# Kernel optimization log

Hardware: AMD Instinct MI355X
Metric: run time of the kernel (lower is better)

## Reference

```python
import jax, jax.numpy as jnp
import numpy as np

N = 16384          # num nodes (adj is dense NxN)
INPUT_DIM = 512
HIDDEN = 128
E_POS = 524288
E_NEG = 524288


def setup_inputs() -> dict:
    key = jax.random.key(0)
    k1, k2, k3, k4, k5, k6, k7 = jax.random.split(key, 7)
    X = jax.random.normal(k1, (N, INPUT_DIM), dtype=jnp.float32)
    adj = jax.random.uniform(k2, (N, N), dtype=jnp.float32)
    train_edges = jax.random.randint(k3, (E_POS, 2), 0, N, dtype=jnp.int64)
    train_false_edges = jax.random.randint(k4, (E_NEG, 2), 0, N, dtype=jnp.int64)
    # parameters (xavier / kaiming scale approximated with uniform bounds)
    b1 = float(np.sqrt(6.0 / (INPUT_DIM + HIDDEN)))
    weight = jax.random.uniform(k5, (INPUT_DIM, HIDDEN), minval=-b1, maxval=b1, dtype=jnp.float32)
    b2 = float(np.sqrt(6.0 / (2 * HIDDEN + HIDDEN)))
    weight_two = jax.random.uniform(k6, (2 * HIDDEN, HIDDEN), minval=-b2, maxval=b2, dtype=jnp.float32)
    b3 = float(np.sqrt(6.0 / HIDDEN) / np.sqrt(2.0))  # kaiming_uniform a=1
    weight_three = jax.random.uniform(k7, (HIDDEN, 1), minval=-b3, maxval=b3, dtype=jnp.float32)
    return {"X": X, "adj": adj, "weight": weight, "weight_two": weight_two,
            "weight_three": weight_three, "train_edges": train_edges,
            "train_false_edges": train_false_edges}


def reference(X, adj, weight, weight_two, weight_three, train_edges, train_false_edges):
    # encode: Z = adj @ (X @ W)
    Z = adj @ (X @ weight)                                  # [N, H]
    edges = jnp.concatenate([train_edges, train_false_edges], axis=0)  # [E, 2]
    # decode: vectorized gather-concat replacing the per-edge Python loop
    z_pair = jnp.concatenate([Z[edges[:, 0]], Z[edges[:, 1]]], axis=1)  # [E, 2H]
    h = jax.nn.relu(z_pair) @ weight_two @ weight_three      # [E, 1]
    return jax.nn.sigmoid(h)
```

## Files before the change

### kernel.cpp

```cpp
#include <hip/hip_runtime.h>


#define N_NODES 16384
#define IN_DIM  512
#define HID     128
#define E_POS_N 524288
#define E_TOT   1048576

typedef __bf16 bf16x8 __attribute__((ext_vector_type(8)));
typedef float  f32x4  __attribute__((ext_vector_type(4)));
typedef unsigned short us8 __attribute__((ext_vector_type(8)));
typedef unsigned short us4 __attribute__((ext_vector_type(4)));

__device__ __forceinline__ bf16x8 ldsb(const void* p){
  return __builtin_bit_cast(bf16x8, *reinterpret_cast<const us8*>(p));
}
__device__ __forceinline__ void gload16(const void* g, void* l){
  __builtin_amdgcn_global_load_lds(
      (const __attribute__((address_space(1))) unsigned int*)g,
      (__attribute__((address_space(3))) unsigned int*)l, 16, 0, 0);
}
__device__ __forceinline__ void gload16nt(const void* g, void* l){
  __builtin_amdgcn_global_load_lds(
      (const __attribute__((address_space(1))) unsigned int*)g,
      (__attribute__((address_space(3))) unsigned int*)l, 16, 0, 2);
}

__device__ __forceinline__ void split8(const float* f, bf16x8& hi, bf16x8& lo){
  unsigned u[8];
#pragma unroll
  for (int i = 0; i < 8; ++i) u[i] = __float_as_uint(f[i]);
  uint4 hv;
  hv.x = __builtin_amdgcn_perm(u[1], u[0], 0x07060302u);
  hv.y = __builtin_amdgcn_perm(u[3], u[2], 0x07060302u);
  hv.z = __builtin_amdgcn_perm(u[5], u[4], 0x07060302u);
  hv.w = __builtin_amdgcn_perm(u[7], u[6], 0x07060302u);
  hi = __builtin_bit_cast(bf16x8, hv);
  bf16x8 lv;
#pragma unroll
  for (int i = 0; i < 8; ++i)
    lv[i] = (__bf16)(f[i] - __uint_as_float(u[i] & 0xFFFF0000u));
  lo = lv;
}

__global__ __launch_bounds__(512) void prep_kernel(const float* __restrict__ W,
                                                   const float* __restrict__ w2,
                                                   const float* __restrict__ w3,
                                                   unsigned short* __restrict__ bfW,
                                                   float* __restrict__ w23){
  const int blk = blockIdx.x, tid = threadIdx.x;
  if (blk < 16){
    const int c = tid & 127, g = tid >> 7;
    float f[8];
#pragma unroll
    for (int j = 0; j < 8; ++j) f[j] = W[(blk * 32 + g * 8 + j) * HID + c];
    bf16x8 hi, lo; split8(f, hi, lo);
    const int sw = (c & 7) << 4;
    char* tb = (char*)bfW + blk * 16384 + c * 128;
    *(us8*)(tb + ((g * 16) ^ sw))      = __builtin_bit_cast(us8, hi);
    *(us8*)(tb + ((64 + g * 16) ^ sw)) = __builtin_bit_cast(us8, lo);
  } else if (tid < 256){
    float acc = 0.f;
#pragma unroll 4
    for (int k = 0; k < HID; ++k) acc = fmaf(w2[tid * HID + k], w3[k], acc);
    w23[tid] = acc;
  }
}

__global__ __launch_bounds__(256) void xw_kernel(const float* __restrict__ X,
                                                 const unsigned short* __restrict__ bfW,
                                                 unsigned short* __restrict__ bfB){
  __shared__ alignas(16) char lds[4][24576];
  const int tid = threadIdx.x, lane = tid & 63, w = tid >> 6;
  const int blk = blockIdx.x;
  const int g = lane >> 4, l15 = lane & 15;

  int aoff[4][2], boffH[2], boffL[2];
#pragma unroll
  for (int m = 0; m < 4; ++m){
    const int r = m * 16 + l15, sw = (r & 7) << 4;
    aoff[m][0] = r * 128 + ((g * 32) ^ sw);
    aoff[m][1] = r * 128 + ((g * 32 + 16) ^ sw);
  }
#pragma unroll
  for (int n = 0; n < 2; ++n){
    const int c = (w & 3) * 32 + n * 16 + l15, sw = (c & 7) << 4;
    boffH[n] = 8192 + c * 128 + ((g * 16) ^ sw);
    boffL[n] = 8192 + c * 128 + ((64 + g * 16) ^ sw);
  }

  const char* xsrc[2];
#pragma unroll
  for (int i = 0; i < 2; ++i){
    const int r = i * 32 + (tid >> 3);
    xsrc[i] = (const char*)X + ((size_t)(blk * 64 + r) * IN_DIM) * 4
            + (((tid & 7) * 16) ^ ((r & 7) << 4));
  }
  const char* bsrc = (const char*)bfW + tid * 16;

#define XSTAGE(buf, tt) do { \
    gload16(xsrc[0] + (tt) * 128, (buf) + tid * 16); \
    gload16(xsrc[1] + (tt) * 128, (buf) + 4096 + tid * 16); \
    gload16(bsrc + (size_t)(tt) * 16384,         (buf) + 8192  + tid * 16); \
    gload16(bsrc + (size_t)(tt) * 16384 + 4096,  (buf) + 12288 + tid * 16); \
    gload16(bsrc + (size_t)(tt) * 16384 + 8192,  (buf) + 16384 + tid * 16); \
    gload16(bsrc + (size_t)(tt) * 16384 + 12288, (buf) + 20480 + tid * 16); \
  } while (0)

  f32x4 acc[4][2] = {};
  auto compute = [&](const char* bp){
    bf16x8 bHv[2], bLv[2];
#pragma unroll
    for (int n = 0; n < 2; ++n){ bHv[n] = ldsb(bp + boffH[n]); bLv[n] = ldsb(bp + boffL[n]); }
#pragma unroll
    for (int m = 0; m < 4; ++m){
      f32x4 v0 = *(const f32x4*)(bp + aoff[m][0]);
      f32x4 v1 = *(const f32x4*)(bp + aoff[m][1]);
      float f[8] = {v0[0], v0[1], v0[2], v0[3], v1[0], v1[1], v1[2], v1[3]};
      bf16x8 aH, aL; split8(f, aH, aL);
      __builtin_amdgcn_s_setprio(1);
#pragma unroll
      for (int n = 0; n < 2; ++n) acc[m][n] = __builtin_amdgcn_mfma_f32_16x16x32_bf16(aH, bHv[n], acc[m][n], 0, 0, 0);
#pragma unroll
      for (int n = 0; n < 2; ++n) acc[m][n] = __builtin_amdgcn_mfma_f32_16x16x32_bf16(aH, bLv[n], acc[m][n], 0, 0, 0);
#pragma unroll
      for (int n = 0; n < 2; ++n) acc[m][n] = __builtin_amdgcn_mfma_f32_16x16x32_bf16(aL, bHv[n], acc[m][n], 0, 0, 0);
      __builtin_amdgcn_s_setprio(0);
    }
  };

  XSTAGE(lds[0], 0); XSTAGE(lds[1], 1); XSTAGE(lds[2], 2);
  asm volatile("s_waitcnt vmcnt(12)" ::: "memory");
  __builtin_amdgcn_s_barrier();

  const int nt = IN_DIM / 32;
#pragma unroll 1
  for (int t = 0; t < nt; ++t){
    char* bp = lds[t & 3];
    if (t + 3 < nt) XSTAGE(lds[(t + 3) & 3], t + 3);
    compute(bp);
    if (t + 3 < nt)      asm volatile("s_waitcnt vmcnt(12)" ::: "memory");
    else if (t + 2 < nt) asm volatile("s_waitcnt vmcnt(6)" ::: "memory");
    else if (t + 1 < nt) asm volatile("s_waitcnt vmcnt(0)" ::: "memory");
    if (t + 1 < nt) __builtin_amdgcn_s_barrier();
  }
#undef XSTAGE

#pragma unroll
  for (int m = 0; m < 4; ++m){
#pragma unroll
    for (int n = 0; n < 2; ++n){
      const int col = (w & 3) * 32 + n * 16 + l15;
      const int T   = 2 * blk + (m >> 1);
      const int g2  = (2 * m + (g >> 1)) & 3;
      const int sw  = (col & 7) << 4;
      char* tb = (char*)bfB + (size_t)T * 16384 + col * 128;
      uint2 hv;
      hv.x = __builtin_amdgcn_perm(__float_as_uint(acc[m][n][1]), __float_as_uint(acc[m][n][0]), 0x07060302u);
      hv.y = __builtin_amdgcn_perm(__float_as_uint(acc[m][n][3]), __float_as_uint(acc[m][n][2]), 0x07060302u);
      us4 lv;
#pragma unroll
      for (int j = 0; j < 4; ++j){
        unsigned u = __float_as_uint(acc[m][n][j]);
        lv[j] = __builtin_bit_cast(unsigned short,
                 (__bf16)(acc[m][n][j] - __uint_as_float(u & 0xFFFF0000u)));
      }
      *(uint2*)(tb + (((g2 * 16) ^ sw) + (g & 1) * 8))      = hv;
      *(uint2*)(tb + (((64 + g2 * 16) ^ sw) + (g & 1) * 8)) = __builtin_bit_cast(uint2, lv);
    }
  }
}

__global__ __launch_bounds__(512, 4) void zgemm_kernel(const float* __restrict__ adj,
                                                       const unsigned short* __restrict__ bfB,
                                                       float* __restrict__ part){
  __shared__ alignas(16) char lds[2][32768];
  const int tid = threadIdx.x, lane = tid & 63, w = tid >> 6;
  const int wm = w >> 1, wn = w & 1;
  const int xcd = blockIdx.x & 7;
  const int s   = xcd & 3;
  const int mt  = ((xcd >> 2) << 6) + (blockIdx.x >> 3);
  const int k0  = s * (N_NODES / 4);
  const int nt  = (N_NODES / 4) / 32;
  const int g = lane >> 4, l15 = lane & 15;

  int aoff[2][2], boffH[4], boffL[4];
#pragma unroll
  for (int m = 0; m < 2; ++m){
    const int r = wm * 32 + m * 16 + l15, sw = (r & 7) << 4;
    aoff[m][0] = r * 128 + ((g * 32) ^ sw);
    aoff[m][1] = r * 128 + ((g * 32 + 16) ^ sw);
  }
#pragma unroll
  for (int n = 0; n < 4; ++n){
    const int c = wn * 64 + n * 16 + l15, sw = (c & 7) << 4;
    boffH[n] = 16384 + c * 128 + ((g * 16) ^ sw);
    boffL[n] = 16384 + c * 128 + ((64 + g * 16) ^ sw);
  }

  const char* asrc[2];
#pragma unroll
  for (int i = 0; i < 2; ++i){
    const int r = i * 64 + (tid >> 3);
    asrc[i] = (const char*)adj + ((size_t)(mt * 128 + r) * N_NODES + k0) * 4
            + (((tid & 7) * 16) ^ ((r & 7) << 4));
  }
  const char* bsrc = (const char*)bfB + (size_t)(k0 >> 5) * 16384 + tid * 16;

#define ZSTAGE(buf, tt) do { \
    gload16nt(asrc[0] + (size_t)(tt) * 128, (buf) + tid * 16); \
    gload16nt(asrc[1] + (size_t)(tt) * 128, (buf) + 8192 + tid * 16); \
    gload16(bsrc + (size_t)(tt) * 16384,        (buf) + 16384 + tid * 16); \
    gload16(bsrc + (size_t)(tt) * 16384 + 8192, (buf) + 24576 + tid * 16); \
  } while (0)

  f32x4 acc[2][4] = {};
  auto compute = [&](const char* bp){
    bf16x8 bHv[4], bLv[4];
#pragma unroll
    for (int n = 0; n < 4; ++n){ bHv[n] = ldsb(bp + boffH[n]); bLv[n] = ldsb(bp + boffL[n]); }
#pragma unroll
    for (int m = 0; m < 2; ++m){
      f32x4 v0 = *(const f32x4*)(bp + aoff[m][0]);
      f32x4 v1 = *(const f32x4*)(bp + aoff[m][1]);
      float f[8] = {v0[0], v0[1], v0[2], v0[3], v1[0], v1[1], v1[2], v1[3]};
      bf16x8 aH, aL; split8(f, aH, aL);
      __builtin_amdgcn_s_setprio(1);
#pragma unroll
      for (int n = 0; n < 4; ++n) acc[m][n] = __builtin_amdgcn_mfma_f32_16x16x32_bf16(aH, bHv[n], acc[m][n], 0, 0, 0);
#pragma unroll
      for (int n = 0; n < 4; ++n) acc[m][n] = __builtin_amdgcn_mfma_f32_16x16x32_bf16(aH, bLv[n], acc[m][n], 0, 0, 0);
#pragma unroll
      for (int n = 0; n < 4; ++n) acc[m][n] = __builtin_amdgcn_mfma_f32_16x16x32_bf16(aL, bHv[n], acc[m][n], 0, 0, 0);
      __builtin_amdgcn_s_setprio(0);
    }
  };

  ZSTAGE(lds[0], 0); ZSTAGE(lds[1], 1);
  asm volatile("s_waitcnt vmcnt(4)" ::: "memory");
  __builtin_amdgcn_s_barrier();
  __builtin_amdgcn_sched_barrier(0);

#pragma unroll 1
  for (int t = 0; t < nt; ++t){
    compute(lds[t & 1]);
    __builtin_amdgcn_sched_barrier(0);
    __builtin_amdgcn_s_barrier();
    if (t + 2 < nt) ZSTAGE(lds[t & 1], t + 2);
    if (t + 1 < nt){
      if (t + 2 < nt) asm volatile("s_waitcnt vmcnt(4)" ::: "memory");
      else            asm volatile("s_waitcnt vmcnt(0)" ::: "memory");
      __builtin_amdgcn_s_barrier();
      __builtin_amdgcn_sched_barrier(0);
    }
  }
#undef ZSTAGE

  float* pb = part + (size_t)s * ((size_t)N_NODES * HID);
  const int row0 = mt * 128 + wm * 32;
  const int col0 = wn * 64;
#pragma unroll
  for (int m = 0; m < 2; ++m){
#pragma unroll
    for (int n = 0; n < 4; ++n){
#pragma unroll
      for (int j = 0; j < 4; ++j){
        const int row = row0 + m * 16 + g * 4 + j;
        const int col = col0 + n * 16 + l15;
        __builtin_nontemporal_store(acc[m][n][j], &pb[(size_t)row * HID + col]);
      }
    }
  }
}

__global__ __launch_bounds__(256) void nodered_kernel(const float* __restrict__ part,
                                                      const float* __restrict__ w23,
                                                      float* __restrict__ aarr,
                                                      float* __restrict__ barr){
  const int lane = threadIdx.x & 63, wv = threadIdx.x >> 6;
  const int n0 = blockIdx.x * 16 + wv * 4;
  const float w1a = w23[lane],       w1b = w23[lane + 64];
  const float w2a = w23[128 + lane], w2b = w23[192 + lane];
  const float* p = part + (size_t)n0 * HID;
  const size_t NH = (size_t)N_NODES * HID;
  float av[4], bv[4];
#pragma unroll
  for (int u = 0; u < 4; ++u){
    float z1 = 0.f, z2 = 0.f;
#pragma unroll
    for (int sI = 0; sI < 4; ++sI){
      z1 += __builtin_nontemporal_load(&p[sI * NH + u * HID + lane]);
      z2 += __builtin_nontemporal_load(&p[sI * NH + u * HID + lane + 64]);
    }
    z1 = fmaxf(z1, 0.f); z2 = fmaxf(z2, 0.f);
    av[u] = z1 * w1a + z2 * w1b;
    bv[u] = z1 * w2a + z2 * w2b;
  }
#pragma unroll
  for (int u = 0; u < 4; ++u){
#pragma unroll
    for (int o = 32; o > 0; o >>= 1){
      av[u] += __shfl_down(av[u], o);
      bv[u] += __shfl_down(bv[u], o);
    }
  }
  if (lane == 0){
#pragma unroll
    for (int u = 0; u < 4; ++u){ aarr[n0 + u] = av[u]; barr[n0 + u] = bv[u]; }
  }
}

__global__ __launch_bounds__(256) void edge_kernel(const int* __restrict__ e0,
                                                   const int* __restrict__ e1,
                                                   const float* __restrict__ aarr,
                                                   const float* __restrict__ barr,
                                                   float* __restrict__ out){
  const int e = (blockIdx.x * 256 + threadIdx.x) * 4;
  const int* ep; int eb;
  if (e < E_POS_N){ ep = e0; eb = e; } else { ep = e1; eb = e - E_POS_N; }
  int4 p0 = *(const int4*)(ep + 2 * eb);
  int4 p1 = *(const int4*)(ep + 2 * eb + 4);
  float4 o;
  o.x = aarr[p0.x] + barr[p0.y];
  o.y = aarr[p0.z] + barr[p0.w];
  o.z = aarr[p1.x] + barr[p1.y];
  o.w = aarr[p1.z] + barr[p1.w];
  o.x = 1.f / (1.f + __expf(-o.x));
  o.y = 1.f / (1.f + __expf(-o.y));
  o.z = 1.f / (1.f + __expf(-o.z));
  o.w = 1.f / (1.f + __expf(-o.w));
  *(float4*)(out + e) = o;
}

extern "C" void kernel_launch(void* const* d_in, const int* in_sizes, int n_in,
                              void* d_out, int out_size, void* d_ws, size_t ws_size,
                              hipStream_t stream){
  const float* X   = (const float*)d_in[0];
  const float* adj = (const float*)d_in[1];
  const float* W   = (const float*)d_in[2];
  const float* W2  = (const float*)d_in[3];
  const float* W3  = (const float*)d_in[4];
  const int*   e0  = (const int*)d_in[5];
  const int*   e1  = (const int*)d_in[6];
  float* out = (float*)d_out;

  char* wsb = (char*)d_ws;
  const size_t MB = 1024 * 1024;
  unsigned short* bfB = (unsigned short*)(wsb);
  unsigned short* bfW = (unsigned short*)(wsb + 8 * MB);
  float* w23  = (float*)(wsb + 8 * MB + 512 * 1024);
  float* aarr = (float*)(wsb + 9 * MB);
  float* barr = (float*)(wsb + 9 * MB + 64 * 1024);
  float* part = (float*)(wsb + 16 * MB);

  hipLaunchKernelGGL(prep_kernel, dim3(17), dim3(512), 0, stream, W, W2, W3, bfW, w23);
  hipLaunchKernelGGL(xw_kernel, dim3(N_NODES / 64), dim3(256), 0, stream, X, bfW, bfB);
  hipLaunchKernelGGL(zgemm_kernel, dim3(512), dim3(512), 0, stream, adj, bfB, part);
  hipLaunchKernelGGL(nodered_kernel, dim3(N_NODES / 16), dim3(256), 0, stream,
                     part, w23, aarr, barr);
  hipLaunchKernelGGL(edge_kernel, dim3(E_TOT / 1024), dim3(256), 0, stream,
                     e0, e1, aarr, barr, out);
}
```

Measured before the change: 286.6 us.

## Deepen zgemm pipeline with 64-wide A stages and 4-slot B ring

Restructures the adj@XW GEMM load pipeline. A tiles now cover 64 k-columns (256-byte rows) double-buffered in two halves, and B tiles use a 4-slot ring prefetched three steps ahead. LDS per block grows from 64KB to 128KB, so occupancy drops from 4 to 2 blocks per CU via launch_bounds. The aim is more bytes in flight and deeper latency hiding for the memory-bound fp32 adj stream, at the cost of fewer resident waves and more complex vmcnt bookkeeping.

```diff
diff --git a/kernel.cpp b/kernel.cpp
--- a/kernel.cpp
+++ b/kernel.cpp
@@ -171,58 +171,67 @@
   }
 }
 
-__global__ __launch_bounds__(512, 4) void zgemm_kernel(const float* __restrict__ adj,
+__global__ __launch_bounds__(512, 2) void zgemm_kernel(const float* __restrict__ adj,
                                                        const unsigned short* __restrict__ bfB,
                                                        float* __restrict__ part){
-  __shared__ alignas(16) char lds[2][32768];
+  __shared__ alignas(16) char lds[131072];
   const int tid = threadIdx.x, lane = tid & 63, w = tid >> 6;
   const int wm = w >> 1, wn = w & 1;
   const int xcd = blockIdx.x & 7;
   const int s   = xcd & 3;
   const int mt  = ((xcd >> 2) << 6) + (blockIdx.x >> 3);
   const int k0  = s * (N_NODES / 4);
-  const int nt  = (N_NODES / 4) / 32;
+  const int NP  = (N_NODES / 4) / 32;
   const int g = lane >> 4, l15 = lane & 15;
 
-  int aoff[2][2], boffH[4], boffL[4];
+  int aoff[2][2];
 #pragma unroll
   for (int m = 0; m < 2; ++m){
     const int r = wm * 32 + m * 16 + l15, sw = (r & 7) << 4;
-    aoff[m][0] = r * 128 + ((g * 32) ^ sw);
-    aoff[m][1] = r * 128 + ((g * 32 + 16) ^ sw);
-  }
+    aoff[m][0] = r * 256 + ((g * 32) ^ sw);
+    aoff[m][1] = aoff[m][0] ^ 16;
+  }
+  int boffH[4], boffL[4];
 #pragma unroll
   for (int n = 0; n < 4; ++n){
     const int c = wn * 64 + n * 16 + l15, sw = (c & 7) << 4;
-    boffH[n] = 16384 + c * 128 + ((g * 16) ^ sw);
-    boffL[n] = 16384 + c * 128 + ((64 + g * 16) ^ sw);
-  }
-
-  const char* asrc[2];
-#pragma unroll
-  for (int i = 0; i < 2; ++i){
-    const int r = i * 64 + (tid >> 3);
+    boffH[n] = c * 128 + ((g * 16) ^ sw);
+    boffL[n] = c * 128 + ((64 + g * 16) ^ sw);
+  }
+
+  const char* asrc[4];
+#pragma unroll
+  for (int i = 0; i < 4; ++i){
+    const int r = i * 32 + (tid >> 4);
     asrc[i] = (const char*)adj + ((size_t)(mt * 128 + r) * N_NODES + k0) * 4
-            + (((tid & 7) * 16) ^ ((r & 7) << 4));
+            + ((tid & 8) << 4) + (((tid & 7) * 16) ^ ((r & 7) << 4));
   }
   const char* bsrc = (const char*)bfB + (size_t)(k0 >> 5) * 16384 + tid * 16;
 
-#define ZSTAGE(buf, tt) do { \
-    gload16nt(asrc[0] + (size_t)(tt) * 128, (buf) + tid * 16); \
-    gload16nt(asrc[1] + (size_t)(tt) * 128, (buf) + 8192 + tid * 16); \
-    gload16(bsrc + (size_t)(tt) * 16384,        (buf) + 16384 + tid * 16); \
-    gload16(bsrc + (size_t)(tt) * 16384 + 8192, (buf) + 24576 + tid * 16); \
+#define STAGE_A(half, ss) do { \
+    const size_t so_ = (size_t)(ss) * 256; \
+    gload16nt(asrc[0] + so_, lds + (half) * 32768 + tid * 16); \
+    gload16nt(asrc[1] + so_, lds + (half) * 32768 + 8192  + tid * 16); \
+    gload16nt(asrc[2] + so_, lds + (half) * 32768 + 16384 + tid * 16); \
+    gload16nt(asrc[3] + so_, lds + (half) * 32768 + 24576 + tid * 16); \
   } while (0)
+#define STAGE_B(i) do { \
+    const char* bs_ = bsrc + (size_t)(i) * 16384; \
+    char* bd_ = lds + 65536 + ((i) & 3) * 16384 + tid * 16; \
+    gload16(bs_, bd_); gload16(bs_ + 8192, bd_ + 8192); \
+  } while (0)
 
   f32x4 acc[2][4] = {};
-  auto compute = [&](const char* bp){
+  auto compute = [&](int ah, int sub, int bslot){
+    const char* ap = lds + ah * 32768 + sub * 128;
+    const char* bp = lds + 65536 + bslot * 16384;
     bf16x8 bHv[4], bLv[4];
 #pragma unroll
     for (int n = 0; n < 4; ++n){ bHv[n] = ldsb(bp + boffH[n]); bLv[n] = ldsb(bp + boffL[n]); }
 #pragma unroll
     for (int m = 0; m < 2; ++m){
-      f32x4 v0 = *(const f32x4*)(bp + aoff[m][0]);
-      f32x4 v1 = *(const f32x4*)(bp + aoff[m][1]);
+      f32x4 v0 = *(const f32x4*)(ap + aoff[m][0]);
+      f32x4 v1 = *(const f32x4*)(ap + aoff[m][1]);
       float f[8] = {v0[0], v0[1], v0[2], v0[3], v1[0], v1[1], v1[2], v1[3]};
       bf16x8 aH, aL; split8(f, aH, aL);
       __builtin_amdgcn_s_setprio(1);
@@ -236,25 +245,33 @@
     }
   };
 
-  ZSTAGE(lds[0], 0); ZSTAGE(lds[1], 1);
-  asm volatile("s_waitcnt vmcnt(4)" ::: "memory");
+  STAGE_A(0, 0);
+  STAGE_B(0); STAGE_B(1); STAGE_B(2);
+  asm volatile("s_waitcnt vmcnt(0)" ::: "memory");
   __builtin_amdgcn_s_barrier();
-  __builtin_amdgcn_sched_barrier(0);
 
 #pragma unroll 1
-  for (int t = 0; t < nt; ++t){
-    compute(lds[t & 1]);
+  for (int p = 0; p < NP; ++p){
+    compute((p >> 1) & 1, p & 1, p & 3);
     __builtin_amdgcn_sched_barrier(0);
     __builtin_amdgcn_s_barrier();
-    if (t + 2 < nt) ZSTAGE(lds[t & 1], t + 2);
-    if (t + 1 < nt){
-      if (t + 2 < nt) asm volatile("s_waitcnt vmcnt(4)" ::: "memory");
-      else            asm volatile("s_waitcnt vmcnt(0)" ::: "memory");
+    if ((p & 1) == 0 && p < NP - 2) STAGE_A(((p >> 1) + 1) & 1, (p >> 1) + 1);
+    if (p + 3 < NP) STAGE_B(p + 3);
+    if (p < NP - 3){
+      if ((p & 1) == 0) asm volatile("s_waitcnt vmcnt(8)" ::: "memory");
+      else              asm volatile("s_waitcnt vmcnt(4)" ::: "memory");
+    } else if (p == NP - 3){
+      asm volatile("s_waitcnt vmcnt(2)" ::: "memory");
+    } else if (p == NP - 2){
+      asm volatile("s_waitcnt vmcnt(0)" ::: "memory");
+    }
+    if (p + 1 < NP){
       __builtin_amdgcn_s_barrier();
       __builtin_amdgcn_sched_barrier(0);
     }
   }
-#undef ZSTAGE
+#undef STAGE_A
+#undef STAGE_B
 
   float* pb = part + (size_t)s * ((size_t)N_NODES * HID);
   const int row0 = mt * 128 + wm * 32;
```

New measurement: 330.9 us. +15.5%, slower.
